# Kernel optimization log

Hardware: AMD Instinct MI355X
Metric: run time of the kernel (lower is better)

Reference implementation:

```python
import jax, jax.numpy as jnp
import numpy as np

N, E, IN, H, C, OUT = 50000, 800000, 128, 4, 32, 40
HID = H * C  # 128


def _layernorm(x, g, b, eps=1e-5):
    mu = x.mean(-1, keepdims=True)
    var = ((x - mu) ** 2).mean(-1, keepdims=True)
    return (x - mu) * jax.lax.rsqrt(var + eps) * g + b


def _gatv2(x, src, dst, Wl, bl, Wr, br, att, bias, heads, ch, concat):
    n = x.shape[0]
    xl = (x @ Wl + bl).reshape(n, heads, ch)  # source-side transform
    xr = (x @ Wr + br).reshape(n, heads, ch)  # target-side transform
    e = jax.nn.leaky_relu(xl[src] + xr[dst], 0.2)          # [E,H,C]
    alpha = jnp.einsum('ehc,hc->eh', e, att)                # [E,H]
    m = jax.ops.segment_max(alpha, dst, num_segments=n)
    m = jnp.where(jnp.isfinite(m), m, 0.0)
    a = jnp.exp(alpha - m[dst])
    denom = jax.ops.segment_sum(a, dst, num_segments=n)
    a = a / (denom[dst] + 1e-16)
    out = jax.ops.segment_sum(xl[src] * a[:, :, None], dst, num_segments=n)  # [N,H,C]
    out = out.reshape(n, heads * ch) if concat else out.mean(1)
    return out + bias


def setup_inputs():
    key = jax.random.key(0)
    ks = jax.random.split(key, 26)
    s = 0.05
    rn = lambda k, sh: jax.random.normal(k, sh, jnp.float32) * s
    inp = {
        'x': jax.random.normal(ks[0], (N, IN), jnp.float32),
        'edge_index': jax.random.randint(ks[1], (2, E), 0, N, jnp.int64),
        'W0': rn(ks[2], (IN, HID)), 'b0': jnp.zeros((HID,), jnp.float32),
        'W1l': rn(ks[3], (IN, HID)), 'b1l': jnp.zeros((HID,), jnp.float32),
        'W1r': rn(ks[4], (IN, HID)), 'b1r': jnp.zeros((HID,), jnp.float32),
        'att1': rn(ks[5], (H, C)), 'bias1': jnp.zeros((HID,), jnp.float32),
        'g1': jnp.ones((HID,), jnp.float32), 'be1': jnp.zeros((HID,), jnp.float32),
        'W2l': rn(ks[6], (HID, HID)), 'b2l': jnp.zeros((HID,), jnp.float32),
        'W2r': rn(ks[7], (HID, HID)), 'b2r': jnp.zeros((HID,), jnp.float32),
        'att2': rn(ks[8], (H, C)), 'bias2': jnp.zeros((HID,), jnp.float32),
        'g2': jnp.ones((HID,), jnp.float32), 'be2': jnp.zeros((HID,), jnp.float32),
        'W3l': rn(ks[9], (HID, OUT)), 'b3l': jnp.zeros((OUT,), jnp.float32),
        'W3r': rn(ks[10], (HID, OUT)), 'b3r': jnp.zeros((OUT,), jnp.float32),
        'att3': rn(ks[11], (1, OUT)), 'bias3': jnp.zeros((OUT,), jnp.float32),
    }
    return inp


def reference(x, edge_index, W0, b0, W1l, b1l, W1r, b1r, att1, bias1, g1, be1,
              W2l, b2l, W2r, b2r, att2, bias2, g2, be2,
              W3l, b3l, W3r, b3r, att3, bias3):
    src, dst = edge_index[0], edge_index[1]
    identity = x @ W0 + b0
    out = _gatv2(x, src, dst, W1l, b1l, W1r, b1r, att1, bias1, H, C, True)
    out = jax.nn.gelu(_layernorm(out, g1, be1), approximate=False)
    x1 = out + identity  # dropout is identity in eval mode
    out = _gatv2(x1, src, dst, W2l, b2l, W2r, b2r, att2, bias2, H, C, True)
    out = jax.nn.gelu(_layernorm(out, g2, be2), approximate=False)
    x2 = out + x1
    return _gatv2(x2, src, dst, W3l, b3l, W3r, b3r, att3, bias3, 1, OUT, False)
```

## Files before the change

kernel.cpp:

```cpp
#include <hip/hip_runtime.h>
#include <hip/hip_bf16.h>

#define NN 50000
#define EE 800000
#define OUTD 40
#define NBUCK 196
#define BCAP 8192
#define ABLKS 400
#define EPB 2000

typedef __attribute__((ext_vector_type(8))) short short8;
typedef __attribute__((ext_vector_type(4))) float floatx4;

__device__ __forceinline__ float bf2f(unsigned short u) {
  union { unsigned int i; float f; } v; v.i = ((unsigned int)u) << 16; return v.f;
}
__device__ __forceinline__ unsigned short f2bf(float f) {
  union { float f; unsigned int i; } v; v.f = f;
  unsigned int x = v.i;
  return (unsigned short)((x + 0x7fffu + ((x >> 16) & 1u)) >> 16);
}
__device__ __forceinline__ float blo(unsigned int u) {
  union { unsigned int i; float f; } v; v.i = u << 16; return v.f;
}
__device__ __forceinline__ float bhi(unsigned int u) {
  union { unsigned int i; float f; } v; v.i = u & 0xffff0000u; return v.f;
}

template <int CTRL>
__device__ __forceinline__ float dpp_add(float x) {
  int y = __builtin_amdgcn_update_dpp(0, __float_as_int(x), CTRL, 0xF, 0xF, true);
  return x + __int_as_float(y);
}

__device__ __forceinline__ float gelu1(float y) {
  float y2 = y * y;
  float z = y * fmaf(0.0356774081f, y2, 0.7978845608f);
  float e = __expf(-2.f * z);
  float r = __builtin_amdgcn_rcpf(1.f + e);
  float th = fmaf(2.f, r, -1.f);
  return y * fmaf(0.5f, th, 0.5f);
}

__device__ __forceinline__ int clampe(int i, int last) {
  int r = i <= last ? i : last;
  return r < 0 ? 0 : r;
}

__device__ __forceinline__ int probe_f32(const void* x) {
  int lane = threadIdx.x & 63;
  unsigned short u = ((const unsigned short*)x)[2 * lane];
  int exf = (u >> 7) & 0xFF;
  unsigned long long b = __ballot((exf >= 100 && exf <= 142) ? 1 : 0);
  return (__popcll(b) >= 48) ? 0 : 1;
}
__device__ __forceinline__ int probe_i64(const void* ei) {
  int lane = threadIdx.x & 63;
  long long v = ((const long long*)ei)[lane];
  unsigned long long b = __ballot((v >= 0 && v < NN) ? 1 : 0);
  return (__popcll(b) >= 48) ? 1 : 0;
}

struct WDesc { const void* W; unsigned short* F; int T; int ncols; };
struct WDescs { WDesc d[7]; int cum[8]; };
struct PCv { const void* s; unsigned short* d; int n; int cap; };
struct PCvs { PCv a[17]; };

__global__ __launch_bounds__(256) void init_kernel(const void* __restrict__ ei,
                                                   const void* __restrict__ x,
                                                   int* __restrict__ flags,
                                                   int* __restrict__ bcur,
                                                   WDescs ds, PCvs P) {
  int b = blockIdx.x;
  int f32 = probe_f32(x);
  if (b < 48) {
    int idx = b * 256 + threadIdx.x;
    if (idx >= 12288) return;
    int mi = 0;
    while (idx >= ds.cum[mi + 1]) mi++;
    int local = idx - ds.cum[mi];
    WDesc d = ds.d[mi];
    int lane = local & 63;
    int rest = local >> 6;
    int t = rest % d.T;
    int kb = rest / d.T;
    int m = lane & 15, quad = lane >> 4;
    int col = t * 16 + m;
    short8 v;
    for (int j = 0; j < 8; ++j) {
      int k = kb * 32 + quad * 8 + j;
      if (col < d.ncols) {
        int off = k * d.ncols + col;
        v[j] = f32 ? (short)f2bf(((const float*)d.W)[off])
                   : (short)((const unsigned short*)d.W)[off];
      } else {
        v[j] = 0;
      }
    }
    *(short8*)(d.F + (size_t)local * 8) = v;
  } else if (b < 65) {
    PCv p = P.a[b - 48];
    for (int i = threadIdx.x; i < p.cap; i += 256) {
      unsigned short o = 0;
      if (i < p.n)
        o = f32 ? f2bf(((const float*)p.s)[i]) : ((const unsigned short*)p.s)[i];
      p.d[i] = o;
    }
  } else {
    for (int i = threadIdx.x; i < NBUCK * 16; i += 256) bcur[i] = 0;
    if (threadIdx.x < 64) {
      int i64 = probe_i64(ei);
      if (threadIdx.x == 0) {
        flags[0] = i64;
        flags[1] = f32;
        flags[2] = 0;
      }
    }
  }
}

struct GSet { const unsigned short* F; const unsigned short* bias; unsigned short* Out; };
struct GArgs { GSet s[3]; };

__device__ __forceinline__ short8 pack_f4(float4 u0, float4 u1) {
  short8 r;
  r[0] = (short)f2bf(u0.x); r[1] = (short)f2bf(u0.y);
  r[2] = (short)f2bf(u0.z); r[3] = (short)f2bf(u0.w);
  r[4] = (short)f2bf(u1.x); r[5] = (short)f2bf(u1.y);
  r[6] = (short)f2bf(u1.z); r[7] = (short)f2bf(u1.w);
  return r;
}

__device__ __forceinline__ void gemm_body(int wave, int lane, const void* __restrict__ A,
                                          int f32, const GArgs& g, int nset, int M,
                                          int T, int ncols) {
  int r0 = wave * 16;
  if (r0 >= M) return;
  int m = lane & 15, quad = lane >> 4;
  short8 a0, a1, a2, a3;
  if (!f32) {
    const unsigned short* ar = (const unsigned short*)A + (size_t)(r0 + m) * 128 + quad * 8;
    a0 = *(const short8*)(ar);
    a1 = *(const short8*)(ar + 32);
    a2 = *(const short8*)(ar + 64);
    a3 = *(const short8*)(ar + 96);
  } else {
    const float* ar = (const float*)A + (size_t)(r0 + m) * 128 + quad * 8;
    a0 = pack_f4(*(const float4*)(ar), *(const float4*)(ar + 4));
    a1 = pack_f4(*(const float4*)(ar + 32), *(const float4*)(ar + 36));
    a2 = pack_f4(*(const float4*)(ar + 64), *(const float4*)(ar + 68));
    a3 = pack_f4(*(const float4*)(ar + 96), *(const float4*)(ar + 100));
  }
  size_t kstride = (size_t)T * 64 * 8;
  for (int si = 0; si < nset; ++si) {
    const unsigned short* F = g.s[si].F;
    const unsigned short* bias = g.s[si].bias;
    unsigned short* Out = g.s[si].Out;
    for (int t = 0; t < T; ++t) {
      floatx4 acc = {0.f, 0.f, 0.f, 0.f};
      const unsigned short* wp = F + ((size_t)t * 64 + lane) * 8;
      acc = __builtin_amdgcn_mfma_f32_16x16x32_bf16(a0, *(const short8*)(wp), acc, 0, 0, 0);
      acc = __builtin_amdgcn_mfma_f32_16x16x32_bf16(a1, *(const short8*)(wp + kstride), acc, 0, 0, 0);
      acc = __builtin_amdgcn_mfma_f32_16x16x32_bf16(a2, *(const short8*)(wp + 2 * kstride), acc, 0, 0, 0);
      acc = __builtin_amdgcn_mfma_f32_16x16x32_bf16(a3, *(const short8*)(wp + 3 * kstride), acc, 0, 0, 0);
      int col = t * 16 + m;
      if (col < ncols) {
        float bb = bf2f(bias[col]);
        for (int r = 0; r < 4; ++r) {
          int row = r0 + quad * 4 + r;
          Out[(size_t)row * ncols + col] = f2bf(acc[r] + bb);
        }
      }
    }
  }
}

__global__ __launch_bounds__(512) void fused_scatter_gemm(
    const void* __restrict__ ei, unsigned int* __restrict__ bedges,
    int* __restrict__ bcur, const void* __restrict__ A,
    const int* __restrict__ flagp, GArgs g, int nset, int M, int T, int ncols) {
  __shared__ int lhist[NBUCK];
  __shared__ int lbase[NBUCK];
  if (blockIdx.x >= ABLKS) {
    int wave = (blockIdx.x - ABLKS) * 8 + (threadIdx.x >> 6);
    gemm_body(wave, threadIdx.x & 63, A, *flagp, g, nset, M, T, ncols);
    return;
  }
  int tid = threadIdx.x;
  if (tid < NBUCK) lhist[tid] = 0;
  int i64 = probe_i64(ei);
  __syncthreads();
  int e0 = blockIdx.x * EPB;
  int e1 = e0 + EPB; if (e1 > EE) e1 = EE;
  for (int e = e0 + tid; e < e1; e += 512) {
    int d = i64 ? (int)((const long long*)ei)[EE + e] : ((const int*)ei)[EE + e];
    d = d < 0 ? 0 : (d >= NN ? NN - 1 : d);
    atomicAdd(&lhist[d >> 8], 1);
  }
  __syncthreads();
  if (tid < NBUCK) {
    int c = lhist[tid];
    lbase[tid] = c ? atomicAdd(&bcur[tid * 16], c) : 0;
    lhist[tid] = 0;
  }
  __syncthreads();
  for (int e = e0 + tid; e < e1; e += 512) {
    int s, d;
    if (i64) {
      s = (int)((const long long*)ei)[e];
      d = (int)((const long long*)ei)[EE + e];
    } else {
      s = ((const int*)ei)[e];
      d = ((const int*)ei)[EE + e];
    }
    s = s < 0 ? 0 : (s >= NN ? NN - 1 : s);
    d = d < 0 ? 0 : (d >= NN ? NN - 1 : d);
    int bin = d >> 8;
    int r = atomicAdd(&lhist[bin], 1);
    int pos = lbase[bin] + r;
    if (pos < BCAP)
      bedges[(size_t)bin * BCAP + pos] =
          ((unsigned int)(d & 0xFF) << 24) | ((unsigned int)s << 8);
  }
}

__global__ __launch_bounds__(512) void fused_sort_gemm(
    const unsigned int* __restrict__ bedges, const int* __restrict__ bcur,
    int* __restrict__ offs, int* __restrict__ src_sorted,
    const void* __restrict__ A, const int* __restrict__ flagp, GArgs g,
    int nset, int M, int T, int ncols) {
  __shared__ int lhist[256];
  __shared__ int lscan[256];
  __shared__ int lbin[256];
  __shared__ int sbase, scount, stotal;
  __shared__ unsigned int le[BCAP];
  __shared__ unsigned short lrank[BCAP];
  if (blockIdx.x >= NBUCK) {
    int wave = (blockIdx.x - NBUCK) * 8 + (threadIdx.x >> 6);
    gemm_body(wave, threadIdx.x & 63, A, *flagp, g, nset, M, T, ncols);
    return;
  }
  int k = blockIdx.x;
  int tid = threadIdx.x;
  if (tid < 256) {
    int c = 0;
    if (tid < NBUCK) {
      int v = bcur[tid * 16];
      c = v < BCAP ? v : BCAP;
    }
    lscan[tid] = c;
  }
  __syncthreads();
  for (int off = 1; off < 256; off <<= 1) {
    int u = 0;
    if (tid < 256 && tid >= off) u = lscan[tid - off];
    __syncthreads();
    if (tid < 256) lscan[tid] += u;
    __syncthreads();
  }
  if (tid == 0) {
    int pb = (k == 0) ? 0 : lscan[k - 1];
    sbase = pb;
    scount = lscan[k] - pb;
    stotal = lscan[NBUCK - 1];
  }
  if (tid < 256) lhist[tid] = 0;
  __syncthreads();
  int base = sbase, count = scount;
  const unsigned int* myb = bedges + (size_t)k * BCAP;
  for (int i = tid; i < count; i += 512) {
    unsigned int pk = myb[i];
    int bin = pk >> 24;
    int r = atomicAdd(&lhist[bin], 1);
    le[i] = pk;
    lrank[i] = (unsigned short)r;
  }
  __syncthreads();
  int hc = 0;
  if (tid < 256) {
    hc = lhist[tid];
    lscan[tid] = hc;
  }
  __syncthreads();
  for (int off = 1; off < 256; off <<= 1) {
    int u = 0;
    if (tid < 256 && tid >= off) u = lscan[tid - off];
    __syncthreads();
    if (tid < 256) lscan[tid] += u;
    __syncthreads();
  }
  if (tid < 256) {
    int binoff = lscan[tid] - hc;
    lbin[tid] = binoff;
    int node = k * 256 + tid;
    if (node < NN) offs[node] = base + binoff;
    if (k == 0 && tid == 0) offs[NN] = stotal;
  }
  __syncthreads();
  for (int i = tid; i < count; i += 512) {
    unsigned int pk = le[i];
    int bin = pk >> 24;
    int pos = base + lbin[bin] + (int)lrank[i];
    src_sorted[pos] = (int)(pk & 0x00FFFF00u);
  }
}

template <int TT, int NCOLS, int WRITEX>
__global__ __launch_bounds__(512) void edge_hid_kernel(
    const unsigned short* __restrict__ xl, const unsigned short* __restrict__ xr,
    const unsigned short* __restrict__ att, const unsigned short* __restrict__ bias,
    const unsigned short* __restrict__ gamma, const unsigned short* __restrict__ beta,
    const unsigned short* __restrict__ resid, unsigned short* __restrict__ xout,
    const int* __restrict__ offs, const int* __restrict__ srcs,
    const unsigned short* __restrict__ Fl, const unsigned short* __restrict__ Fr,
    const unsigned short* __restrict__ bl, const unsigned short* __restrict__ br,
    unsigned short* __restrict__ outl, unsigned short* __restrict__ outr) {
  __shared__ unsigned short sA[16 * 136];
  const int wid = threadIdx.x >> 6;
  int wpair = blockIdx.x * 8 + wid;
  int lane = threadIdx.x & 63;
  int half = lane >> 5;
  int wv = wpair * 2 + half;
  int hl = lane & 31;
  int sub = hl >> 4;
  int cb = (hl & 15) * 16;
  int beg = offs[wv], end = offs[wv + 1], last = end - 1;
  int iters = (end - beg + 1) >> 1;
  int oi = __shfl_xor(iters, 32);
  int maxit = __builtin_amdgcn_readfirstlane(iters > oi ? iters : oi);
  const char* xlb = (const char*)xl;
  int c0 = hl * 4;
  uint2 rr = *(const uint2*)(resid + (size_t)wv * 128 + c0);
  uint4 xr8 = *(const uint4*)((const char*)xr + (size_t)wv * 256 + cb);
  float rx0 = blo(xr8.x), rx1 = bhi(xr8.x), rx2 = blo(xr8.y), rx3 = bhi(xr8.y);
  float rx4 = blo(xr8.z), rx5 = bhi(xr8.z), rx6 = blo(xr8.w), rx7 = bhi(xr8.w);
  uint4 at8 = *(const uint4*)((const char*)att + cb);
  float a0 = blo(at8.x), a1 = bhi(at8.x), a2 = blo(at8.y), a3 = bhi(at8.y);
  float a4 = blo(at8.z), a5 = bhi(at8.z), a6 = blo(at8.w), a7 = bhi(at8.w);
  float acc0 = 0.f, acc1 = 0.f, acc2 = 0.f, acc3 = 0.f;
  float acc4 = 0.f, acc5 = 0.f, acc6 = 0.f, acc7 = 0.f, den = 0.f;
  int ir = beg + sub;
  int o_cur = srcs[clampe(ir, last)];
  int o_nxt = srcs[clampe(ir + 2, last)];
  uint4 u = *(const uint4*)(xlb + (o_cur + cb));
  for (int it = 0; it < maxit; ++it) {
    int o_p = srcs[clampe(ir + 4, last)];
    uint4 un = *(const uint4*)(xlb + (o_nxt + cb));
    float mk = (ir <= last) ? 1.f : 0.f;
    ir += 2;
    float x0 = blo(u.x), x1 = bhi(u.x), x2 = blo(u.y), x3 = bhi(u.y);
    float x4 = blo(u.z), x5 = bhi(u.z), x6 = blo(u.w), x7 = bhi(u.w);
    float t0 = x0 + rx0, t1 = x1 + rx1, t2 = x2 + rx2, t3 = x3 + rx3;
    float t4 = x4 + rx4, t5 = x5 + rx5, t6 = x6 + rx6, t7 = x7 + rx7;
    float pa = a0 * t0;
    pa = fmaf(a1, t1, pa); pa = fmaf(a2, t2, pa); pa = fmaf(a3, t3, pa);
    pa = fmaf(a4, t4, pa); pa = fmaf(a5, t5, pa); pa = fmaf(a6, t6, pa); pa = fmaf(a7, t7, pa);
    float pb = a0 * fabsf(t0);
    pb = fmaf(a1, fabsf(t1), pb); pb = fmaf(a2, fabsf(t2), pb); pb = fmaf(a3, fabsf(t3), pb);
    pb = fmaf(a4, fabsf(t4), pb); pb = fmaf(a5, fabsf(t5), pb);
    pb = fmaf(a6, fabsf(t6), pb); pb = fmaf(a7, fabsf(t7), pb);
    float p = fmaf(0.4f, pb, 0.6f * pa);
    p = dpp_add<0xB1>(p);
    p = dpp_add<0x4E>(p);
    float w = __expf(fminf(p, 60.f)) * mk;
    den += w;
    acc0 = fmaf(w, x0, acc0); acc1 = fmaf(w, x1, acc1);
    acc2 = fmaf(w, x2, acc2); acc3 = fmaf(w, x3, acc3);
    acc4 = fmaf(w, x4, acc4); acc5 = fmaf(w, x5, acc5);
    acc6 = fmaf(w, x6, acc6); acc7 = fmaf(w, x7, acc7);
    u = un;
    o_nxt = o_p;
  }
  den += __shfl_xor(den, 16);
  acc0 += __shfl_xor(acc0, 16); acc1 += __shfl_xor(acc1, 16);
  acc2 += __shfl_xor(acc2, 16); acc3 += __shfl_xor(acc3, 16);
  acc4 += __shfl_xor(acc4, 16); acc5 += __shfl_xor(acc5, 16);
  acc6 += __shfl_xor(acc6, 16); acc7 += __shfl_xor(acc7, 16);
  int srcLane = (half << 5) + (hl >> 1);
  float b0 = __shfl(acc0, srcLane), b1 = __shfl(acc1, srcLane);
  float b2 = __shfl(acc2, srcLane), b3 = __shfl(acc3, srcLane);
  float h4 = __shfl(acc4, srcLane), h5 = __shfl(acc5, srcLane);
  float h6 = __shfl(acc6, srcLane), h7 = __shfl(acc7, srcLane);
  float dn = __shfl(den, srcLane);
  bool hi = (hl & 1) != 0;
  float v0 = hi ? h4 : b0, v1 = hi ? h5 : b1, v2 = hi ? h6 : b2, v3 = hi ? h7 : b3;
  float inv = __builtin_amdgcn_rcpf(dn + 1e-16f);
  uint2 bb = *(const uint2*)(bias + c0);
  float o0 = v0 * inv + blo(bb.x), o1 = v1 * inv + bhi(bb.x);
  float o2 = v2 * inv + blo(bb.y), o3 = v3 * inv + bhi(bb.y);
  float s = (o0 + o1) + (o2 + o3);
  for (int k = 1; k < 32; k <<= 1) s += __shfl_xor(s, k);
  float mu = s * (1.f / 128.f);
  float d0 = o0 - mu, d1 = o1 - mu, d2 = o2 - mu, d3 = o3 - mu;
  float q = (d0 * d0 + d1 * d1) + (d2 * d2 + d3 * d3);
  for (int k = 1; k < 32; k <<= 1) q += __shfl_xor(q, k);
  float rstd = rsqrtf(q * (1.f / 128.f) + 1e-5f);
  uint2 gg = *(const uint2*)(gamma + c0);
  uint2 be = *(const uint2*)(beta + c0);
  float y0 = d0 * rstd * blo(gg.x) + blo(be.x);
  float y1 = d1 * rstd * bhi(gg.x) + bhi(be.x);
  float y2 = d2 * rstd * blo(gg.y) + blo(be.y);
  float y3 = d3 * rstd * bhi(gg.y) + bhi(be.y);
  y0 = gelu1(y0); y1 = gelu1(y1); y2 = gelu1(y2); y3 = gelu1(y3);
  y0 += blo(rr.x); y1 += bhi(rr.x); y2 += blo(rr.y); y3 += bhi(rr.y);
  uint2 pk;
  pk.x = (unsigned int)f2bf(y0) | ((unsigned int)f2bf(y1) << 16);
  pk.y = (unsigned int)f2bf(y2) | ((unsigned int)f2bf(y3) << 16);
  if (WRITEX) *(uint2*)(xout + (size_t)wv * 128 + c0) = pk;

  int lrow = wid * 2 + half;
  *(uint2*)(&sA[lrow * 136 + c0]) = pk;
  __syncthreads();
  int m = lane & 15, quad = lane >> 4;
  const unsigned short* arow = sA + m * 136 + quad * 8;
  short8 A0 = *(const short8*)(arow);
  short8 A1 = *(const short8*)(arow + 32);
  short8 A2 = *(const short8*)(arow + 64);
  short8 A3 = *(const short8*)(arow + 96);
  const size_t kst = (size_t)TT * 64 * 8;
  const int rowbase = blockIdx.x * 16;
  constexpr int PER = (2 * TT) / 8;
#pragma unroll
  for (int jj = 0; jj < PER; ++jj) {
    int j = wid * PER + jj;
    bool isr = j >= TT;
    const unsigned short* F = isr ? Fr : Fl;
    const unsigned short* bs = isr ? br : bl;
    unsigned short* Out = isr ? outr : outl;
    int t = isr ? j - TT : j;
    floatx4 acc = {0.f, 0.f, 0.f, 0.f};
    const unsigned short* wp = F + ((size_t)t * 64 + lane) * 8;
    acc = __builtin_amdgcn_mfma_f32_16x16x32_bf16(A0, *(const short8*)(wp), acc, 0, 0, 0);
    acc = __builtin_amdgcn_mfma_f32_16x16x32_bf16(A1, *(const short8*)(wp + kst), acc, 0, 0, 0);
    acc = __builtin_amdgcn_mfma_f32_16x16x32_bf16(A2, *(const short8*)(wp + 2 * kst), acc, 0, 0, 0);
    acc = __builtin_amdgcn_mfma_f32_16x16x32_bf16(A3, *(const short8*)(wp + 3 * kst), acc, 0, 0, 0);
    int col = t * 16 + m;
    float bbv = bf2f(bs[col]);
#pragma unroll
    for (int r = 0; r < 4; ++r)
      Out[(size_t)(rowbase + quad * 4 + r) * NCOLS + col] = f2bf(acc[r] + bbv);
  }
}

__global__ __launch_bounds__(256) void edge_out_kernel(
    const unsigned short* __restrict__ xl, const unsigned short* __restrict__ xr,
    const unsigned short* __restrict__ att, const unsigned short* __restrict__ bias,
    void* __restrict__ out, const int* __restrict__ flagp,
    const int* __restrict__ offs, const int* __restrict__ srcs) {
  int wv = blockIdx.x * 4 + (threadIdx.x >> 6);
  if (wv >= NN) return;
  int lane = threadIdx.x & 63;
  int oct = lane >> 3;
  int cb = (lane & 7) * 16;
  int beg = __builtin_amdgcn_readfirstlane(offs[wv]);
  int last = __builtin_amdgcn_readfirstlane(offs[wv + 1]) - 1;
  const char* xlb = (const char*)xl;
  uint4 xr8 = *(const uint4*)((const char*)xr + (size_t)wv * 128 + cb);
  float rx0 = blo(xr8.x), rx1 = bhi(xr8.x), rx2 = blo(xr8.y), rx3 = bhi(xr8.y);
  float rx4 = blo(xr8.z), rx5 = bhi(xr8.z), rx6 = blo(xr8.w), rx7 = bhi(xr8.w);
  uint4 at8 = *(const uint4*)((const char*)att + cb);
  float a0 = blo(at8.x), a1 = bhi(at8.x), a2 = blo(at8.y), a3 = bhi(at8.y);
  float a4 = blo(at8.z), a5 = bhi(at8.z), a6 = blo(at8.w), a7 = bhi(at8.w);
  float acc0 = 0.f, acc1 = 0.f, acc2 = 0.f, acc3 = 0.f;
  float acc4 = 0.f, acc5 = 0.f, acc6 = 0.f, acc7 = 0.f, den = 0.f;
  int ir = beg + oct;
  int o_cur = srcs[clampe(ir, last)];
  int o_nxt = srcs[clampe(ir + 8, last)];
  uint4 u = *(const uint4*)(xlb + ((o_cur >> 1) + cb));
  for (int e = beg; e <= last; e += 8) {
    int o_p = srcs[clampe(ir + 16, last)];
    uint4 un = *(const uint4*)(xlb + ((o_nxt >> 1) + cb));
    float mk = (ir <= last) ? 1.f : 0.f;
    ir += 8;
    float x0 = blo(u.x), x1 = bhi(u.x), x2 = blo(u.y), x3 = bhi(u.y);
    float x4 = blo(u.z), x5 = bhi(u.z), x6 = blo(u.w), x7 = bhi(u.w);
    float t0 = x0 + rx0, t1 = x1 + rx1, t2 = x2 + rx2, t3 = x3 + rx3;
    float t4 = x4 + rx4, t5 = x5 + rx5, t6 = x6 + rx6, t7 = x7 + rx7;
    float pa = a0 * t0;
    pa = fmaf(a1, t1, pa); pa = fmaf(a2, t2, pa); pa = fmaf(a3, t3, pa);
    pa = fmaf(a4, t4, pa); pa = fmaf(a5, t5, pa); pa = fmaf(a6, t6, pa); pa = fmaf(a7, t7, pa);
    float pb = a0 * fabsf(t0);
    pb = fmaf(a1, fabsf(t1), pb); pb = fmaf(a2, fabsf(t2), pb); pb = fmaf(a3, fabsf(t3), pb);
    pb = fmaf(a4, fabsf(t4), pb); pb = fmaf(a5, fabsf(t5), pb);
    pb = fmaf(a6, fabsf(t6), pb); pb = fmaf(a7, fabsf(t7), pb);
    float p = fmaf(0.4f, pb, 0.6f * pa);
    p = dpp_add<0xB1>(p);
    p = dpp_add<0x4E>(p);
    p = dpp_add<0x141>(p);
    float w = __expf(fminf(p, 60.f)) * mk;
    den += w;
    acc0 = fmaf(w, x0, acc0); acc1 = fmaf(w, x1, acc1);
    acc2 = fmaf(w, x2, acc2); acc3 = fmaf(w, x3, acc3);
    acc4 = fmaf(w, x4, acc4); acc5 = fmaf(w, x5, acc5);
    acc6 = fmaf(w, x6, acc6); acc7 = fmaf(w, x7, acc7);
    u = un;
    o_nxt = o_p;
  }
  den += __shfl_xor(den, 8);  den += __shfl_xor(den, 16);  den += __shfl_xor(den, 32);
  acc0 += __shfl_xor(acc0, 8); acc0 += __shfl_xor(acc0, 16); acc0 += __shfl_xor(acc0, 32);
  acc1 += __shfl_xor(acc1, 8); acc1 += __shfl_xor(acc1, 16); acc1 += __shfl_xor(acc1, 32);
  acc2 += __shfl_xor(acc2, 8); acc2 += __shfl_xor(acc2, 16); acc2 += __shfl_xor(acc2, 32);
  acc3 += __shfl_xor(acc3, 8); acc3 += __shfl_xor(acc3, 16); acc3 += __shfl_xor(acc3, 32);
  acc4 += __shfl_xor(acc4, 8); acc4 += __shfl_xor(acc4, 16); acc4 += __shfl_xor(acc4, 32);
  acc5 += __shfl_xor(acc5, 8); acc5 += __shfl_xor(acc5, 16); acc5 += __shfl_xor(acc5, 32);
  acc6 += __shfl_xor(acc6, 8); acc6 += __shfl_xor(acc6, 16); acc6 += __shfl_xor(acc6, 32);
  acc7 += __shfl_xor(acc7, 8); acc7 += __shfl_xor(acc7, 16); acc7 += __shfl_xor(acc7, 32);
  float inv = __builtin_amdgcn_rcpf(den + 1e-16f);
  if (lane < 5) {
    uint4 bb = *(const uint4*)((const char*)bias + cb);
    float v0 = acc0 * inv + blo(bb.x), v1 = acc1 * inv + bhi(bb.x);
    float v2 = acc2 * inv + blo(bb.y), v3 = acc3 * inv + bhi(bb.y);
    float v4 = acc4 * inv + blo(bb.z), v5 = acc5 * inv + bhi(bb.z);
    float v6 = acc6 * inv + blo(bb.w), v7 = acc7 * inv + bhi(bb.w);
    int c0 = lane * 8;
    if (*flagp) {
      float* op = (float*)out + (size_t)wv * OUTD + c0;
      float4 f0 = {v0, v1, v2, v3};
      float4 f1 = {v4, v5, v6, v7};
      *(float4*)(op) = f0;
      *(float4*)(op + 4) = f1;
    } else {
      uint4 pk;
      pk.x = (unsigned int)f2bf(v0) | ((unsigned int)f2bf(v1) << 16);
      pk.y = (unsigned int)f2bf(v2) | ((unsigned int)f2bf(v3) << 16);
      pk.z = (unsigned int)f2bf(v4) | ((unsigned int)f2bf(v5) << 16);
      pk.w = (unsigned int)f2bf(v6) | ((unsigned int)f2bf(v7) << 16);
      *(uint4*)((unsigned short*)out + (size_t)wv * OUTD + c0) = pk;
    }
  }
}

extern "C" void kernel_launch(void* const* d_in, const int* in_sizes, int n_in,
                              void* d_out, int out_size, void* d_ws, size_t ws_size,
                              hipStream_t stream) {
  const void* x = d_in[0];
  const void* ei = d_in[1];

  char* ws = (char*)d_ws;
  size_t o = 0;
  auto alloc = [&](size_t bytes) {
    void* p = ws + o;
    o = (o + bytes + 255) & ~(size_t)255;
    return p;
  };
  int* flags = (int*)alloc(256);
  int* src_sorted = (int*)alloc((size_t)EE * 4);
  int* offs = (int*)alloc((size_t)(NN + 1) * 4);
  int* bcur = (int*)alloc((size_t)NBUCK * 16 * 4);
  unsigned int* bedges = (unsigned int*)alloc((size_t)NBUCK * BCAP * 4);
  unsigned short* F_W0 = (unsigned short*)alloc(2048 * 16);
  unsigned short* F_W1l = (unsigned short*)alloc(2048 * 16);
  unsigned short* F_W1r = (unsigned short*)alloc(2048 * 16);
  unsigned short* F_W2l = (unsigned short*)alloc(2048 * 16);
  unsigned short* F_W2r = (unsigned short*)alloc(2048 * 16);
  unsigned short* F_W3l = (unsigned short*)alloc(1024 * 16);
  unsigned short* F_W3r = (unsigned short*)alloc(1024 * 16);
  unsigned short* pblk = (unsigned short*)alloc(4096);
  unsigned short* ident = (unsigned short*)alloc((size_t)NN * 128 * 2);
  unsigned short* bxlA = (unsigned short*)alloc((size_t)NN * 128 * 2);
  unsigned short* bxrA = (unsigned short*)alloc((size_t)NN * 128 * 2);
  unsigned short* bxlB = (unsigned short*)alloc((size_t)NN * 128 * 2);
  unsigned short* bxrB = (unsigned short*)alloc((size_t)NN * 128 * 2);
  (void)ws_size;

  unsigned short* pb0 = pblk;
  unsigned short* pb1l = pblk + 128;
  unsigned short* pb1r = pblk + 256;
  unsigned short* patt1 = pblk + 384;
  unsigned short* pbias1 = pblk + 512;
  unsigned short* pg1 = pblk + 640;
  unsigned short* pbe1 = pblk + 768;
  unsigned short* pb2l = pblk + 896;
  unsigned short* pb2r = pblk + 1024;
  unsigned short* patt2 = pblk + 1152;
  unsigned short* pbias2 = pblk + 1280;
  unsigned short* pg2 = pblk + 1408;
  unsigned short* pbe2 = pblk + 1536;
  unsigned short* pb3l = pblk + 1664;
  unsigned short* pb3r = pblk + 1728;
  unsigned short* patt3 = pblk + 1792;
  unsigned short* pbias3 = pblk + 1856;

  WDescs wd;
  wd.d[0] = {d_in[2], F_W0, 8, 128};
  wd.d[1] = {d_in[4], F_W1l, 8, 128};
  wd.d[2] = {d_in[6], F_W1r, 8, 128};
  wd.d[3] = {d_in[12], F_W2l, 8, 128};
  wd.d[4] = {d_in[14], F_W2r, 8, 128};
  wd.d[5] = {d_in[20], F_W3l, 4, 40};
  wd.d[6] = {d_in[22], F_W3r, 4, 40};
  int cum[8] = {0, 2048, 4096, 6144, 8192, 10240, 11264, 12288};
  for (int i = 0; i < 8; ++i) wd.cum[i] = cum[i];
  PCvs P;
  P.a[0] = {d_in[3], pb0, 128, 128};
  P.a[1] = {d_in[5], pb1l, 128, 128};
  P.a[2] = {d_in[7], pb1r, 128, 128};
  P.a[3] = {d_in[8], patt1, 128, 128};
  P.a[4] = {d_in[9], pbias1, 128, 128};
  P.a[5] = {d_in[10], pg1, 128, 128};
  P.a[6] = {d_in[11], pbe1, 128, 128};
  P.a[7] = {d_in[13], pb2l, 128, 128};
  P.a[8] = {d_in[15], pb2r, 128, 128};
  P.a[9] = {d_in[16], patt2, 128, 128};
  P.a[10] = {d_in[17], pbias2, 128, 128};
  P.a[11] = {d_in[18], pg2, 128, 128};
  P.a[12] = {d_in[19], pbe2, 128, 128};
  P.a[13] = {d_in[21], pb3l, 40, 64};
  P.a[14] = {d_in[23], pb3r, 40, 64};
  P.a[15] = {d_in[24], patt3, 40, 64};
  P.a[16] = {d_in[25], pbias3, 40, 64};
  init_kernel<<<66, 256, 0, stream>>>(ei, x, flags, bcur, wd, P);

  const int* fx = flags + 1;
  const int gb8 = (NN + 127) / 128;
  const int eb = (NN + 3) / 4;
  const int eb16 = NN / 16;

  GArgs gi; gi.s[0] = {F_W0, pb0, ident};
  gi.s[1] = {nullptr, nullptr, nullptr}; gi.s[2] = {nullptr, nullptr, nullptr};
  fused_scatter_gemm<<<ABLKS + gb8, 512, 0, stream>>>(ei, bedges, bcur, x, fx, gi, 1,
                                                      NN, 8, 128);

  GArgs g1a; g1a.s[0] = {F_W1l, pb1l, bxlA}; g1a.s[1] = {F_W1r, pb1r, bxrA};
  g1a.s[2] = {nullptr, nullptr, nullptr};
  fused_sort_gemm<<<NBUCK + gb8, 512, 0, stream>>>(bedges, bcur, offs, src_sorted, x,
                                                   fx, g1a, 2, NN, 8, 128);

  edge_hid_kernel<8, 128, 1><<<eb16, 512, 0, stream>>>(
      bxlA, bxrA, patt1, pbias1, pg1, pbe1, ident, ident, offs, src_sorted,
      F_W2l, F_W2r, pb2l, pb2r, bxlB, bxrB);

  edge_hid_kernel<4, 64, 0><<<eb16, 512, 0, stream>>>(
      bxlB, bxrB, patt2, pbias2, pg2, pbe2, ident, ident, offs, src_sorted,
      F_W3l, F_W3r, pb3l, pb3r, bxlA, bxrA);

  edge_out_kernel<<<eb, 256, 0, stream>>>(bxlA, bxrA, patt3, pbias3, d_out, fx, offs,
                                          src_sorted);
}
```

Baseline: 295.9 us.

## Fold init work into scatter kernel and merge identity GEMM into sort GEMM

Removes the separate init kernel. Its weight repacking, parameter conversion and flag probing now run in extra blocks of the scatter kernel, and the bucket counters are cleared with a memset. The identity projection GEMM moves out of the scatter kernel into the sort+GEMM kernel as a third weight set, so x is read once for all three projections. This removes one launch and the serialized small init pass, at the cost of a memset node and a heavier GEMM phase in the sort kernel.

```diff
diff --git a/kernel.cpp b/kernel.cpp
--- a/kernel.cpp
+++ b/kernel.cpp
@@ -65,59 +65,6 @@
 struct WDescs { WDesc d[7]; int cum[8]; };
 struct PCv { const void* s; unsigned short* d; int n; int cap; };
 struct PCvs { PCv a[17]; };
-
-__global__ __launch_bounds__(256) void init_kernel(const void* __restrict__ ei,
-                                                   const void* __restrict__ x,
-                                                   int* __restrict__ flags,
-                                                   int* __restrict__ bcur,
-                                                   WDescs ds, PCvs P) {
-  int b = blockIdx.x;
-  int f32 = probe_f32(x);
-  if (b < 48) {
-    int idx = b * 256 + threadIdx.x;
-    if (idx >= 12288) return;
-    int mi = 0;
-    while (idx >= ds.cum[mi + 1]) mi++;
-    int local = idx - ds.cum[mi];
-    WDesc d = ds.d[mi];
-    int lane = local & 63;
-    int rest = local >> 6;
-    int t = rest % d.T;
-    int kb = rest / d.T;
-    int m = lane & 15, quad = lane >> 4;
-    int col = t * 16 + m;
-    short8 v;
-    for (int j = 0; j < 8; ++j) {
-      int k = kb * 32 + quad * 8 + j;
-      if (col < d.ncols) {
-        int off = k * d.ncols + col;
-        v[j] = f32 ? (short)f2bf(((const float*)d.W)[off])
-                   : (short)((const unsigned short*)d.W)[off];
-      } else {
-        v[j] = 0;
-      }
-    }
-    *(short8*)(d.F + (size_t)local * 8) = v;
-  } else if (b < 65) {
-    PCv p = P.a[b - 48];
-    for (int i = threadIdx.x; i < p.cap; i += 256) {
-      unsigned short o = 0;
-      if (i < p.n)
-        o = f32 ? f2bf(((const float*)p.s)[i]) : ((const unsigned short*)p.s)[i];
-      p.d[i] = o;
-    }
-  } else {
-    for (int i = threadIdx.x; i < NBUCK * 16; i += 256) bcur[i] = 0;
-    if (threadIdx.x < 64) {
-      int i64 = probe_i64(ei);
-      if (threadIdx.x == 0) {
-        flags[0] = i64;
-        flags[1] = f32;
-        flags[2] = 0;
-      }
-    }
-  }
-}
 
 struct GSet { const unsigned short* F; const unsigned short* bias; unsigned short* Out; };
 struct GArgs { GSet s[3]; };
@@ -175,15 +122,59 @@
   }
 }
 
-__global__ __launch_bounds__(512) void fused_scatter_gemm(
-    const void* __restrict__ ei, unsigned int* __restrict__ bedges,
-    int* __restrict__ bcur, const void* __restrict__ A,
-    const int* __restrict__ flagp, GArgs g, int nset, int M, int T, int ncols) {
+__global__ __launch_bounds__(512) void fused_scatter_init(
+    const void* __restrict__ ei, const void* __restrict__ x,
+    unsigned int* __restrict__ bedges, int* __restrict__ bcur,
+    int* __restrict__ flags, WDescs ds, PCvs P) {
   __shared__ int lhist[NBUCK];
   __shared__ int lbase[NBUCK];
   if (blockIdx.x >= ABLKS) {
-    int wave = (blockIdx.x - ABLKS) * 8 + (threadIdx.x >> 6);
-    gemm_body(wave, threadIdx.x & 63, A, *flagp, g, nset, M, T, ncols);
+    int b = blockIdx.x - ABLKS;
+    int tid = threadIdx.x;
+    int f32 = probe_f32(x);
+    if (b < 24) {
+      int idx = b * 512 + tid;
+      if (idx >= 12288) return;
+      int mi = 0;
+      while (idx >= ds.cum[mi + 1]) mi++;
+      int local = idx - ds.cum[mi];
+      WDesc d = ds.d[mi];
+      int lane = local & 63;
+      int rest = local >> 6;
+      int t = rest % d.T;
+      int kb = rest / d.T;
+      int m = lane & 15, quad = lane >> 4;
+      int col = t * 16 + m;
+      short8 v;
+      for (int j = 0; j < 8; ++j) {
+        int k = kb * 32 + quad * 8 + j;
+        if (col < d.ncols) {
+          int off = k * d.ncols + col;
+          v[j] = f32 ? (short)f2bf(((const float*)d.W)[off])
+                     : (short)((const unsigned short*)d.W)[off];
+        } else {
+          v[j] = 0;
+        }
+      }
+      *(short8*)(d.F + (size_t)local * 8) = v;
+    } else if (b < 41) {
+      PCv p = P.a[b - 24];
+      for (int i = tid; i < p.cap; i += 512) {
+        unsigned short o = 0;
+        if (i < p.n)
+          o = f32 ? f2bf(((const float*)p.s)[i]) : ((const unsigned short*)p.s)[i];
+        p.d[i] = o;
+      }
+    } else {
+      if (tid < 64) {
+        int i64 = probe_i64(ei);
+        if (tid == 0) {
+          flags[0] = i64;
+          flags[1] = f32;
+          flags[2] = 0;
+        }
+      }
+    }
     return;
   }
   int tid = threadIdx.x;
@@ -609,22 +600,22 @@
   P.a[14] = {d_in[23], pb3r, 40, 64};
   P.a[15] = {d_in[24], patt3, 40, 64};
   P.a[16] = {d_in[25], pbias3, 40, 64};
-  init_kernel<<<66, 256, 0, stream>>>(ei, x, flags, bcur, wd, P);
 
   const int* fx = flags + 1;
   const int gb8 = (NN + 127) / 128;
   const int eb = (NN + 3) / 4;
   const int eb16 = NN / 16;
 
-  GArgs gi; gi.s[0] = {F_W0, pb0, ident};
-  gi.s[1] = {nullptr, nullptr, nullptr}; gi.s[2] = {nullptr, nullptr, nullptr};
-  fused_scatter_gemm<<<ABLKS + gb8, 512, 0, stream>>>(ei, bedges, bcur, x, fx, gi, 1,
-                                                      NN, 8, 128);
-
-  GArgs g1a; g1a.s[0] = {F_W1l, pb1l, bxlA}; g1a.s[1] = {F_W1r, pb1r, bxrA};
-  g1a.s[2] = {nullptr, nullptr, nullptr};
+  hipMemsetAsync(bcur, 0, (size_t)NBUCK * 16 * 4, stream);
+
+  fused_scatter_init<<<ABLKS + 42, 512, 0, stream>>>(ei, x, bedges, bcur, flags, wd, P);
+
+  GArgs g1a;
+  g1a.s[0] = {F_W0, pb0, ident};
+  g1a.s[1] = {F_W1l, pb1l, bxlA};
+  g1a.s[2] = {F_W1r, pb1r, bxrA};
   fused_sort_gemm<<<NBUCK + gb8, 512, 0, stream>>>(bedges, bcur, offs, src_sorted, x,
-                                                   fx, g1a, 2, NN, 8, 128);
+                                                   fx, g1a, 3, NN, 8, 128);
 
   edge_hid_kernel<8, 128, 1><<<eb16, 512, 0, stream>>>(
       bxlA, bxrA, patt1, pbias1, pg1, pbe1, ident, ident, offs, src_sorted,
```

Result: faster. 288.1 us (-2.6%).
